# Performance work log

Hardware: AMD Instinct MI355X
Metric: run time of the kernel (lower is better)

## Reference

```python
import jax, jax.numpy as jnp
import numpy as np

B = 4096
C3 = 1.0 / np.sqrt(3.0)
# Wigner 3j tensors for the l<=1 paths (e3nn real basis)
W3J_000 = jnp.ones((1, 1, 1), dtype=jnp.float32)
W3J_110 = (jnp.eye(3) * C3).reshape(3, 3, 1).astype(jnp.float32)
W3J_011 = (jnp.eye(3) * C3).reshape(1, 3, 3).astype(jnp.float32)
W3J_101 = (jnp.eye(3) * C3).reshape(3, 1, 3).astype(jnp.float32)


def setup_inputs() -> dict:
    key = jax.random.key(0)
    ks = jax.random.split(key, 10)
    n = lambda k, s: jax.random.normal(k, s, dtype=jnp.float32)
    return {
        "feat": n(ks[0], (B, 320)),        # 128x0e + 64x1o
        "node_emb": n(ks[1], (B, 128)),
        # o3.Linear(irreps_node -> irreps_block): one mixing matrix per l
        "W0": n(ks[2], (128, 16)),          # 0e: 128 -> 16
        "W1": n(ks[3], (64, 16)),           # 1o: 64 -> 16
        # lin_weight MLP: 128 -> 64 -> 36864
        "lw1": n(ks[4], (128, 64)) * 0.1, "lb1": jnp.zeros((64,), jnp.float32),
        "lw2": n(ks[5], (64, 36864)) * 0.1, "lb2": jnp.zeros((36864,), jnp.float32),
        # lin_bias MLP: 128 -> 64 -> 1280
        "bw1": n(ks[6], (128, 64)) * 0.1, "bb1": jnp.zeros((64,), jnp.float32),
        "bw2": n(ks[7], (64, 1280)) * 0.1, "bb2": jnp.zeros((1280,), jnp.float32),
    }


def _path(x, wpath, w3j, bias):
    # x: [B, mul_in, dim_in]; wpath: [B, mul_in, u, v]; w3j: [i, j, k]
    r = jnp.einsum('bwuv,bwk->buvk', wpath, x)
    if bias is not None:
        r = r + bias[..., None]
    out = jnp.einsum('ijk,buvk->buivj', w3j, r) / x.shape[1]
    b, u, i, v, j = out.shape
    return out.reshape(b, u * i, v * j)


def reference(feat, node_emb, W0, W1, lw1, lb1, lw2, lb2, bw1, bb1, bw2, bb2):
    bn = feat.shape[0]
    # split feat into irreps: 128x0e | 64x1o
    s = feat[:, :128].reshape(bn, 128, 1)
    v = feat[:, 128:].reshape(bn, 64, 3)
    # o3.Linear with e3nn path normalization 1/sqrt(fan_in)
    x0 = jnp.einsum('buk,uv->bvk', s, W0) / np.sqrt(128.0)  # [B,16,1]
    x1 = jnp.einsum('buk,uv->bvk', v, W1) / np.sqrt(64.0)   # [B,16,3]
    # per-sample path weights and biases
    w = jax.nn.silu(node_emb @ lw1 + lb1) @ lw2 + lb2        # [B,36864]
    bb = jax.nn.silu(node_emb @ bw1 + bb1) @ bw2 + bb2       # [B,1280]
    # weight slices per instruction (flat layout matches instruction order)
    w00 = w[:, :16384].reshape(bn, 16, 32, 32)               # 0e -> (0e,0e)
    w11 = w[:, 16384:20480].reshape(bn, 16, 16, 16)          # 0e -> (1o,1o)
    w01 = w[:, 20480:28672].reshape(bn, 16, 32, 16)          # 1o -> (0e,1o)
    w10 = w[:, 28672:36864].reshape(bn, 16, 16, 32)          # 1o -> (1o,0e)
    b00 = bb[:, :1024].reshape(bn, 32, 32)
    b11 = bb[:, 1024:1280].reshape(bn, 16, 16)
    blk00 = _path(x0, w00, W3J_000, b00)   # [B,32,32]
    blk11 = _path(x0, w11, W3J_110, b11)   # [B,48,48]
    blk01 = _path(x1, w01, W3J_011, None)  # [B,32,48]
    blk10 = _path(x1, w10, W3J_101, None)  # [B,48,32]
    top = jnp.concatenate([blk00, blk01], axis=-1)
    bot = jnp.concatenate([blk10, blk11], axis=-1)
    return jnp.concatenate([top, bot], axis=-2)  # [B,80,80]
```

## Files before the change

kernel.cpp:

```cpp
#include <hip/hip_runtime.h>
#include <hip/hip_bf16.h>
#include <math.h>


typedef short bf16x8 __attribute__((ext_vector_type(8)));
typedef float f32x4 __attribute__((ext_vector_type(4)));

static __device__ __forceinline__ short f2bf(float f) {
  unsigned u = __builtin_bit_cast(unsigned, f);
  u = u + 0x7fffu + ((u >> 16) & 1u);
  return (short)(u >> 16);
}

__global__ void k_transpose(const float* __restrict__ lw2, short* __restrict__ lw2f) {
  __shared__ float tile[64][65];
  int n0 = blockIdx.x * 64;
  int t = threadIdx.x;
#pragma unroll
  for (int k = 0; k < 16; ++k) {
    int idx = k * 256 + t;
    int c = idx >> 6, j = idx & 63;
    tile[c][j] = lw2[(size_t)c * 36864 + n0 + j];
  }
  __syncthreads();
#pragma unroll
  for (int k = 0; k < 16; ++k) {
    int idx = k * 256 + t;
    int e = idx & 7, l = (idx >> 3) & 63, half = (idx >> 9) & 1, nbl = idx >> 10;
    int q = l >> 4, colr = l & 15;
    int j = nbl * 16 + colr;
    int c = half * 32 + q * 8 + e;
    size_t nb = (size_t)(n0 >> 4) + nbl;
    lw2f[((nb * 2 + half) * 64 + l) * 8 + e] = f2bf(tile[c][j]);
  }
}

__global__ void k_bias(const float* __restrict__ bw2, const float* __restrict__ lb2,
                       const float* __restrict__ bb2,
                       short* __restrict__ bbf00, short* __restrict__ bbf11,
                       short* __restrict__ bbf01, short* __restrict__ bbf10) {
  int i = blockIdx.x * 256 + threadIdx.x;
  if (i < 98304) {
    int uvb = i / 1536, r = i % 1536;
    int kk = r >> 9, l = (r >> 3) & 63, e = r & 7;
    int q = l >> 4, col = l & 15;
    int uv = uvb * 16 + col, k = kk * 32 + q * 8 + e;
    float v = 0.0f;
    if (k < 64) v = bw2[k * 1280 + uv];
    else if (k < 80) v = lb2[(k - 64) * 1024 + uv];
    else if (k == 80) v = bb2[uv];
    bbf00[i] = f2bf(v);
  } else if (i < 122880) {
    int j = i - 98304;
    int uvb = j / 1536, r = j % 1536;
    int kk = r >> 9, l = (r >> 3) & 63, e = r & 7;
    int q = l >> 4, col = l & 15;
    int uv = uvb * 16 + col, k = kk * 32 + q * 8 + e;
    float v = 0.0f;
    if (k < 64) v = bw2[k * 1280 + 1024 + uv];
    else if (k < 80) v = lb2[16384 + (k - 64) * 256 + uv];
    else if (k == 80) v = bb2[1024 + uv];
    bbf11[j] = f2bf(v);
  } else if (i < 139264) {
    int j = i - 122880;
    int uvb = j >> 9, r = j & 511;
    int l = (r >> 3) & 63, e = r & 7;
    int q = l >> 4, col = l & 15;
    int uv = uvb * 16 + col, k = q * 8 + e;
    bbf01[j] = (k < 16) ? f2bf(lb2[20480 + k * 512 + uv]) : (short)0;
  } else if (i < 155648) {
    int j = i - 139264;
    int uvb = j >> 9, r = j & 511;
    int l = (r >> 3) & 63, e = r & 7;
    int q = l >> 4, col = l & 15;
    int uv = uvb * 16 + col, k = q * 8 + e;
    bbf10[j] = (k < 16) ? f2bf(lb2[28672 + k * 512 + uv]) : (short)0;
  }
}

__global__ void k_samples(const float* __restrict__ feat, const float* __restrict__ ne,
                          const float* __restrict__ W0, const float* __restrict__ W1,
                          const float* __restrict__ lw1, const float* __restrict__ lb1,
                          const float* __restrict__ bw1, const float* __restrict__ bb1,
                          float* __restrict__ H, float* __restrict__ H2,
                          float* __restrict__ X0, float* __restrict__ X1) {
  int b = blockIdx.x;
  int t = threadIdx.x;
  __shared__ float sne[128];
  __shared__ float sf[320];
  if (t < 128) sne[t] = ne[(size_t)b * 128 + t];
  for (int i = t; i < 320; i += 192) sf[i] = feat[(size_t)b * 320 + i];
  __syncthreads();
  if (t < 64) {
    float a = lb1[t];
    for (int k = 0; k < 128; ++k) a += sne[k] * lw1[k * 64 + t];
    H[(size_t)b * 64 + t] = a / (1.0f + expf(-a));
  } else if (t < 128) {
    int c = t - 64;
    float a = bb1[c];
    for (int k = 0; k < 128; ++k) a += sne[k] * bw1[k * 64 + c];
    H2[(size_t)b * 64 + c] = a / (1.0f + expf(-a));
  } else if (t < 144) {
    int v = t - 128;
    float a = 0.0f;
    for (int u = 0; u < 128; ++u) a += sf[u] * W0[u * 16 + v];
    X0[(size_t)b * 16 + v] = a * 0.08838834764831845f;
  } else {
    int idx = t - 144, v = idx / 3, j = idx % 3;
    float a = 0.0f;
    for (int u = 0; u < 64; ++u) a += sf[128 + u * 3 + j] * W1[u * 16 + v];
    X1[(size_t)b * 48 + v * 3 + j] = a * 0.125f;
  }
}

__global__ void k_q(const float* __restrict__ H, const float* __restrict__ H2,
                    const float* __restrict__ X0, const float* __restrict__ X1,
                    short* __restrict__ QF, short* __restrict__ AbF,
                    short* __restrict__ A1F) {
  int bid = blockIdx.x;
  int g16 = bid >> 3, part = bid & 7;
  int b0 = g16 * 16;
  int t = threadIdx.x;
  __shared__ float sH[16][64];
  __shared__ float sH2[16][64];
  __shared__ float sX0[16][16];
  __shared__ float sX1[16][48];
  for (int i = t; i < 1024; i += 256) {
    sH [i >> 6][i & 63] = H [(size_t)(b0 + (i >> 6)) * 64 + (i & 63)];
    sH2[i >> 6][i & 63] = H2[(size_t)(b0 + (i >> 6)) * 64 + (i & 63)];
  }
  sX0[t >> 4][t & 15] = X0[(size_t)(b0 + (t >> 4)) * 16 + (t & 15)];
  for (int i = t; i < 768; i += 256)
    sX1[i / 48][i % 48] = X1[(size_t)(b0 + i / 48) * 48 + (i % 48)];
  __syncthreads();
#pragma unroll
  for (int it = 0; it < 16; ++it) {
    int i = part * 4096 + it * 256 + t;
    int p = i >> 13, rem = i & 8191;
    int kk = rem >> 8, lane = (rem >> 2) & 63, e2 = (rem & 3) << 1;
    int cc = lane & 15, q = lane >> 4;
    int k = kk * 32 + q * 8 + e2;
    int w = k >> 6, c = k & 63;
    float xw = (p == 0) ? sX0[cc][w] : sX1[cc][w * 3 + (p - 1)];
    unsigned lo = (unsigned short)f2bf(sH[cc][c] * xw);
    unsigned hi = (unsigned short)f2bf(sH[cc][c + 1] * xw);
    ((unsigned*)QF)[(size_t)g16 * 32768 + i] = lo | (hi << 16);
  }
  if (part == 0) {
    for (int i = t; i < 1536; i += 256) {
      int kk = i >> 9, lane = (i >> 3) & 63, e = i & 7;
      int cc = lane & 15, q = lane >> 4;
      int k = kk * 32 + q * 8 + e;
      float v = 0.0f;
      if (k < 64) v = sH2[cc][k];
      else if (k < 80) v = sX0[cc][k - 64];
      else if (k == 80) v = 1.0f;
      AbF[(size_t)g16 * 1536 + i] = f2bf(v);
    }
  } else if (part == 1) {
    for (int i = t; i < 1536; i += 256) {
      int j = i >> 9, r = i & 511;
      int lane = r >> 3, e = r & 7;
      int cc = lane & 15, q = lane >> 4;
      int k = q * 8 + e;
      A1F[(size_t)g16 * 1536 + i] = (k < 16) ? f2bf(sX1[cc][k * 3 + j]) : (short)0;
    }
  }
}

template <int NP, int N, int NB16, int NS16>
static __device__ __forceinline__ void mm_stream(
    const short* __restrict__ LW2F, const short* __restrict__ sQ0,
    int uvb, int lane8, f32x4 (&acc)[NP][N]) {
  auto bptr = [&](int kk, int i) -> const bf16x8* {
    return (const bf16x8*)(LW2F +
        ((size_t)(NB16 + (kk >> 1) * NS16 + uvb + i) * 2 + (kk & 1)) * 512 + lane8);
  };
  bf16x8 B[2][N];
#pragma unroll
  for (int d = 0; d < 2; ++d)
#pragma unroll
    for (int i = 0; i < N; ++i) B[d][i] = *bptr(d, i);
#pragma unroll
  for (int kk = 0; kk < 32; ++kk) {
    const int d = kk & 1;
    bf16x8 A[NP];
#pragma unroll
    for (int p = 0; p < NP; ++p)
      A[p] = *(const bf16x8*)(sQ0 + p * 16384 + kk * 512 + lane8);
#pragma unroll
    for (int i = 0; i < N; ++i)
#pragma unroll
      for (int p = 0; p < NP; ++p)
        acc[p][i] = __builtin_amdgcn_mfma_f32_16x16x32_bf16(A[p], B[d][i], acc[p][i], 0, 0, 0);
    if (kk + 2 < 32) {
#pragma unroll
      for (int i = 0; i < N; ++i) B[d][i] = *bptr(kk + 2, i);
    }
  }
}

template <int NP, int N, int NBIAS>
static __device__ __forceinline__ void mm_bias(
    const short* __restrict__ BBF, const short* __restrict__ Ab0, int astride,
    int uvb, int lane8, f32x4 (&acc)[NP][N]) {
#pragma unroll
  for (int kk = 0; kk < NBIAS; ++kk)
#pragma unroll
    for (int i = 0; i < N; ++i) {
      const bf16x8 Bx = *(const bf16x8*)(BBF + (size_t)((uvb + i) * NBIAS + kk) * 512 + lane8);
#pragma unroll
      for (int p = 0; p < NP; ++p) {
        const bf16x8 Ap = *(const bf16x8*)(Ab0 + p * astride + kk * 512 + lane8);
        acc[p][i] = __builtin_amdgcn_mfma_f32_16x16x32_bf16(Ap, Bx, acc[p][i], 0, 0, 0);
      }
    }
}

__global__ __launch_bounds__(1024, 1)
__attribute__((amdgpu_num_vgpr(128)))
void k_main(
    const short* __restrict__ LW2F,
    const short* __restrict__ BBF00, const short* __restrict__ BBF11,
    const short* __restrict__ BBF01, const short* __restrict__ BBF10,
    const short* __restrict__ QF, const short* __restrict__ AbF,
    const short* __restrict__ A1F, float* __restrict__ out) {
  constexpr float S00 = 0.0625f;
  constexpr float S3 = 0.036084391824351614f;

  int bidx = blockIdx.x;
  int xslot = bidx & 7;
  int h = xslot >> 2;
  int s = (xslot & 3) + 4 * (bidx >> 3);
  int b0 = s << 5;
  int t = threadIdx.x;
  int lane = t & 63, slot = t >> 6;
  int col = lane & 15, q = lane >> 4;
  int lane8 = lane * 8;

  __shared__ short sQ[4 * 16384];
  __shared__ short sAb[2 * 1536];
  __shared__ short sA1[6 * 512];

  for (int i = t; i < 384; i += 1024) {
    int g = i >= 192, r = i - g * 192;
    ((uint4*)(sAb + g * 1536))[r] =
        ((const uint4*)(AbF + (size_t)(s * 2 + g) * 1536))[r];
  }
  for (int i = t; i < 384; i += 1024) {
    int jp = i >> 6, r = i & 63;
    int j = jp >> 1, g = jp & 1;
    ((uint4*)(sA1 + jp * 512))[r] =
        ((const uint4*)(A1F + ((size_t)(s * 2 + g) * 3 + j) * 512))[r];
  }
  for (int i = t; i < 4096; i += 1024) {
    int pl = i >> 11, r = i & 2047;
    const uint4* src = (const uint4*)(QF + (size_t)(s * 2 + pl) * 65536);
    ((uint4*)sQ)[pl * 2048 + r] = src[r];
  }
  __syncthreads();

  {
    int uvb = h * 32 + slot * 2;
    f32x4 acc[2][2] = {};
    mm_stream<2, 2, 0, 64>(LW2F, sQ, uvb, lane8, acc);
    mm_bias<2, 2, 3>(BBF00, sAb, 1536, uvb, lane8, acc);
#pragma unroll
    for (int g = 0; g < 2; ++g)
#pragma unroll
      for (int i = 0; i < 2; ++i)
#pragma unroll
        for (int ii = 0; ii < 4; ++ii) {
          size_t ob = (size_t)(b0 + g * 16 + q * 4 + ii) * 6400;
          int uv = (uvb + i) * 16 + col;
          out[ob + (uv >> 5) * 80 + (uv & 31)] = acc[g][i][ii] * S00;
        }
  }
  if (slot < 8) {
    int uvb = h * 8 + slot;
    f32x4 acc[2][1] = {};
    mm_stream<2, 1, 1024, 16>(LW2F, sQ, uvb, lane8, acc);
    mm_bias<2, 1, 3>(BBF11, sAb, 1536, uvb, lane8, acc);
#pragma unroll
    for (int g = 0; g < 2; ++g)
#pragma unroll
      for (int ii = 0; ii < 4; ++ii) {
        size_t ob = (size_t)(b0 + g * 16 + q * 4 + ii) * 6400;
        int uv = uvb * 16 + col;
        float val = acc[g][0][ii] * S3;
        int u = uv >> 4, v = uv & 15;
        float* p = out + ob + (size_t)(32 + 3 * u) * 80 + (32 + 3 * v);
        p[0] = val;   p[1] = 0.f;   p[2] = 0.f;
        p[80] = 0.f;  p[81] = val;  p[82] = 0.f;
        p[160] = 0.f; p[161] = 0.f; p[162] = val;
      }
  }

  __syncthreads();
  for (int i = t; i < 8192; i += 1024) {
    int pl = i >> 11, r = i & 2047;
    const uint4* src = (const uint4*)(QF +
        ((size_t)(s * 2 + (pl & 1)) * 4 + 1 + (pl >> 1)) * 16384);
    ((uint4*)sQ)[pl * 2048 + r] = src[r];
  }
  __syncthreads();
  {
    int uvb = h * 16 + slot;
    {
      f32x4 acc[4][1] = {};
      mm_stream<4, 1, 1280, 32>(LW2F, sQ, uvb, lane8, acc);
      mm_bias<4, 1, 1>(BBF01, sA1, 512, uvb, lane8, acc);
#pragma unroll
      for (int p = 0; p < 4; ++p)
#pragma unroll
        for (int ii = 0; ii < 4; ++ii) {
          int j = p >> 1, g = p & 1;
          size_t ob = (size_t)(b0 + g * 16 + q * 4 + ii) * 6400;
          int uv = uvb * 16 + col;
          out[ob + (uv >> 4) * 80 + 32 + 3 * (uv & 15) + j] = acc[p][0][ii] * S3;
        }
    }
    {
      f32x4 acc[4][1] = {};
      mm_stream<4, 1, 1792, 32>(LW2F, sQ, uvb, lane8, acc);
      mm_bias<4, 1, 1>(BBF10, sA1, 512, uvb, lane8, acc);
#pragma unroll
      for (int p = 0; p < 4; ++p)
#pragma unroll
        for (int ii = 0; ii < 4; ++ii) {
          int j = p >> 1, g = p & 1;
          size_t ob = (size_t)(b0 + g * 16 + q * 4 + ii) * 6400;
          int uv = uvb * 16 + col;
          out[ob + (size_t)(32 + 3 * (uv >> 5) + j) * 80 + (uv & 31)] = acc[p][0][ii] * S3;
        }
    }
  }

  __syncthreads();
  for (int i = t; i < 4096; i += 1024) {
    int pl = i >> 11, r = i & 2047;
    const uint4* src = (const uint4*)(QF + ((size_t)(s * 2 + pl) * 4 + 3) * 16384);
    ((uint4*)sQ)[pl * 2048 + r] = src[r];
  }
  __syncthreads();
  {
    int uvb = h * 16 + slot;
    {
      f32x4 acc[2][1] = {};
      mm_stream<2, 1, 1280, 32>(LW2F, sQ, uvb, lane8, acc);
      mm_bias<2, 1, 1>(BBF01, sA1 + 4 * 512, 512, uvb, lane8, acc);
#pragma unroll
      for (int g = 0; g < 2; ++g)
#pragma unroll
        for (int ii = 0; ii < 4; ++ii) {
          size_t ob = (size_t)(b0 + g * 16 + q * 4 + ii) * 6400;
          int uv = uvb * 16 + col;
          out[ob + (uv >> 4) * 80 + 32 + 3 * (uv & 15) + 2] = acc[g][0][ii] * S3;
        }
    }
    {
      f32x4 acc[2][1] = {};
      mm_stream<2, 1, 1792, 32>(LW2F, sQ, uvb, lane8, acc);
      mm_bias<2, 1, 1>(BBF10, sA1 + 4 * 512, 512, uvb, lane8, acc);
#pragma unroll
      for (int g = 0; g < 2; ++g)
#pragma unroll
        for (int ii = 0; ii < 4; ++ii) {
          size_t ob = (size_t)(b0 + g * 16 + q * 4 + ii) * 6400;
          int uv = uvb * 16 + col;
          out[ob + (size_t)(32 + 3 * (uv >> 5) + 2) * 80 + (uv & 31)] = acc[g][0][ii] * S3;
        }
    }
  }
}

extern "C" void kernel_launch(void* const* d_in, const int* in_sizes, int n_in,
                              void* d_out, int out_size, void* d_ws, size_t ws_size,
                              hipStream_t stream) {
  const float* feat = (const float*)d_in[0];
  const float* ne   = (const float*)d_in[1];
  const float* W0   = (const float*)d_in[2];
  const float* W1   = (const float*)d_in[3];
  const float* lw1  = (const float*)d_in[4];
  const float* lb1  = (const float*)d_in[5];
  const float* lw2  = (const float*)d_in[6];
  const float* lb2  = (const float*)d_in[7];
  const float* bw1  = (const float*)d_in[8];
  const float* bb1  = (const float*)d_in[9];
  const float* bw2  = (const float*)d_in[10];
  const float* bb2  = (const float*)d_in[11];

  char* ws = (char*)d_ws;
  short* LW2F  = (short*)ws; ws += (size_t)36864 * 64 * 2;
  short* BBF00 = (short*)ws; ws += (size_t)98304 * 2;
  short* BBF11 = (short*)ws; ws += (size_t)24576 * 2;
  short* BBF01 = (short*)ws; ws += (size_t)16384 * 2;
  short* BBF10 = (short*)ws; ws += (size_t)16384 * 2;
  float* H  = (float*)ws;   ws += (size_t)4096 * 64 * 4;
  float* H2 = (float*)ws;   ws += (size_t)4096 * 64 * 4;
  float* X0 = (float*)ws;   ws += (size_t)4096 * 16 * 4;
  float* X1 = (float*)ws;   ws += (size_t)4096 * 48 * 4;
  short* QF  = (short*)ws;  ws += (size_t)256 * 65536 * 2;
  short* AbF = (short*)ws;  ws += (size_t)256 * 1536 * 2;
  short* A1F = (short*)ws;  ws += (size_t)256 * 1536 * 2;
  (void)ws_size; (void)in_sizes; (void)n_in; (void)out_size;

  hipLaunchKernelGGL(k_transpose, dim3(576), dim3(256), 0, stream, lw2, LW2F);
  hipLaunchKernelGGL(k_bias, dim3(608), dim3(256), 0, stream, bw2, lb2, bb2,
                     BBF00, BBF11, BBF01, BBF10);
  hipLaunchKernelGGL(k_samples, dim3(4096), dim3(192), 0, stream,
                     feat, ne, W0, W1, lw1, lb1, bw1, bb1, H, H2, X0, X1);
  hipLaunchKernelGGL(k_q, dim3(2048), dim3(256), 0, stream,
                     H, H2, X0, X1, QF, AbF, A1F);
  hipLaunchKernelGGL(k_main, dim3(256), dim3(1024), 0, stream,
                     LW2F, BBF00, BBF11, BBF01, BBF10, QF, AbF, A1F, (float*)d_out);
}
```

Before: 142.1 us.

## Split main kernel into separate l=0-input and l=1-input path kernels

Splits the monolithic main kernel into two launches. The first handles the 00 and 11 paths with 16-sample tiles over 512 blocks and a smaller shared-memory footprint. The second handles the 01 and 10 paths with the original 32-sample tiling. This is meant to raise parallelism and occupancy for the first phase and drop the mid-kernel reload barrier. The cost is an extra kernel launch and halved reuse of streamed LW2F weights per block in the first phase.

```diff
diff --git a/kernel.cpp b/kernel.cpp
--- a/kernel.cpp
+++ b/kernel.cpp
@@ -217,15 +217,70 @@
     }
 }
 
-__global__ __launch_bounds__(1024, 1)
-__attribute__((amdgpu_num_vgpr(128)))
-void k_main(
+__global__ __launch_bounds__(1024, 1) void k_mainA(
     const short* __restrict__ LW2F,
     const short* __restrict__ BBF00, const short* __restrict__ BBF11,
+    const short* __restrict__ QF, const short* __restrict__ AbF,
+    float* __restrict__ out) {
+  constexpr float S00 = 0.0625f;
+  constexpr float S3 = 0.036084391824351614f;
+
+  int bidx = blockIdx.x;
+  int xslot = bidx & 7;
+  int h = xslot >> 2;
+  int tile = (xslot & 3) + 4 * (bidx >> 3);
+  int b0 = tile << 4;
+  int t = threadIdx.x;
+  int lane = t & 63, slot = t >> 6;
+  int col = lane & 15, q = lane >> 4;
+  int lane8 = lane * 8;
+
+  __shared__ short sQ[16384];
+  __shared__ short sAb[1536];
+
+  for (int i = t; i < 2048; i += 1024)
+    ((uint4*)sQ)[i] = ((const uint4*)(QF + (size_t)tile * 65536))[i];
+  if (t < 192) ((uint4*)sAb)[t] = ((const uint4*)(AbF + (size_t)tile * 1536))[t];
+  __syncthreads();
+
+  {
+    int uvb = h * 32 + slot * 2;
+    f32x4 acc[1][2] = {};
+    mm_stream<1, 2, 0, 64>(LW2F, sQ, uvb, lane8, acc);
+    mm_bias<1, 2, 3>(BBF00, sAb, 1536, uvb, lane8, acc);
+#pragma unroll
+    for (int i = 0; i < 2; ++i)
+#pragma unroll
+      for (int ii = 0; ii < 4; ++ii) {
+        size_t ob = (size_t)(b0 + q * 4 + ii) * 6400;
+        int uv = (uvb + i) * 16 + col;
+        out[ob + (uv >> 5) * 80 + (uv & 31)] = acc[0][i][ii] * S00;
+      }
+  }
+  if (slot < 8) {
+    int uvb = h * 8 + slot;
+    f32x4 acc[1][1] = {};
+    mm_stream<1, 1, 1024, 16>(LW2F, sQ, uvb, lane8, acc);
+    mm_bias<1, 1, 3>(BBF11, sAb, 1536, uvb, lane8, acc);
+#pragma unroll
+    for (int ii = 0; ii < 4; ++ii) {
+      size_t ob = (size_t)(b0 + q * 4 + ii) * 6400;
+      int uv = uvb * 16 + col;
+      float val = acc[0][0][ii] * S3;
+      int u = uv >> 4, v = uv & 15;
+      float* p = out + ob + (size_t)(32 + 3 * u) * 80 + (32 + 3 * v);
+      p[0] = val;   p[1] = 0.f;   p[2] = 0.f;
+      p[80] = 0.f;  p[81] = val;  p[82] = 0.f;
+      p[160] = 0.f; p[161] = 0.f; p[162] = val;
+    }
+  }
+}
+
+__global__ __launch_bounds__(1024, 1) void k_mainB(
+    const short* __restrict__ LW2F,
     const short* __restrict__ BBF01, const short* __restrict__ BBF10,
-    const short* __restrict__ QF, const short* __restrict__ AbF,
-    const short* __restrict__ A1F, float* __restrict__ out) {
-  constexpr float S00 = 0.0625f;
+    const short* __restrict__ QF, const short* __restrict__ A1F,
+    float* __restrict__ out) {
   constexpr float S3 = 0.036084391824351614f;
 
   int bidx = blockIdx.x;
@@ -239,64 +294,14 @@
   int lane8 = lane * 8;
 
   __shared__ short sQ[4 * 16384];
-  __shared__ short sAb[2 * 1536];
   __shared__ short sA1[6 * 512];
 
-  for (int i = t; i < 384; i += 1024) {
-    int g = i >= 192, r = i - g * 192;
-    ((uint4*)(sAb + g * 1536))[r] =
-        ((const uint4*)(AbF + (size_t)(s * 2 + g) * 1536))[r];
-  }
   for (int i = t; i < 384; i += 1024) {
     int jp = i >> 6, r = i & 63;
     int j = jp >> 1, g = jp & 1;
     ((uint4*)(sA1 + jp * 512))[r] =
         ((const uint4*)(A1F + ((size_t)(s * 2 + g) * 3 + j) * 512))[r];
   }
-  for (int i = t; i < 4096; i += 1024) {
-    int pl = i >> 11, r = i & 2047;
-    const uint4* src = (const uint4*)(QF + (size_t)(s * 2 + pl) * 65536);
-    ((uint4*)sQ)[pl * 2048 + r] = src[r];
-  }
-  __syncthreads();
-
-  {
-    int uvb = h * 32 + slot * 2;
-    f32x4 acc[2][2] = {};
-    mm_stream<2, 2, 0, 64>(LW2F, sQ, uvb, lane8, acc);
-    mm_bias<2, 2, 3>(BBF00, sAb, 1536, uvb, lane8, acc);
-#pragma unroll
-    for (int g = 0; g < 2; ++g)
-#pragma unroll
-      for (int i = 0; i < 2; ++i)
-#pragma unroll
-        for (int ii = 0; ii < 4; ++ii) {
-          size_t ob = (size_t)(b0 + g * 16 + q * 4 + ii) * 6400;
-          int uv = (uvb + i) * 16 + col;
-          out[ob + (uv >> 5) * 80 + (uv & 31)] = acc[g][i][ii] * S00;
-        }
-  }
-  if (slot < 8) {
-    int uvb = h * 8 + slot;
-    f32x4 acc[2][1] = {};
-    mm_stream<2, 1, 1024, 16>(LW2F, sQ, uvb, lane8, acc);
-    mm_bias<2, 1, 3>(BBF11, sAb, 1536, uvb, lane8, acc);
-#pragma unroll
-    for (int g = 0; g < 2; ++g)
-#pragma unroll
-      for (int ii = 0; ii < 4; ++ii) {
-        size_t ob = (size_t)(b0 + g * 16 + q * 4 + ii) * 6400;
-        int uv = uvb * 16 + col;
-        float val = acc[g][0][ii] * S3;
-        int u = uv >> 4, v = uv & 15;
-        float* p = out + ob + (size_t)(32 + 3 * u) * 80 + (32 + 3 * v);
-        p[0] = val;   p[1] = 0.f;   p[2] = 0.f;
-        p[80] = 0.f;  p[81] = val;  p[82] = 0.f;
-        p[160] = 0.f; p[161] = 0.f; p[162] = val;
-      }
-  }
-
-  __syncthreads();
   for (int i = t; i < 8192; i += 1024) {
     int pl = i >> 11, r = i & 2047;
     const uint4* src = (const uint4*)(QF +
@@ -412,6 +417,8 @@
                      feat, ne, W0, W1, lw1, lb1, bw1, bb1, H, H2, X0, X1);
   hipLaunchKernelGGL(k_q, dim3(2048), dim3(256), 0, stream,
                      H, H2, X0, X1, QF, AbF, A1F);
-  hipLaunchKernelGGL(k_main, dim3(256), dim3(1024), 0, stream,
-                     LW2F, BBF00, BBF11, BBF01, BBF10, QF, AbF, A1F, (float*)d_out);
-}
+  hipLaunchKernelGGL(k_mainA, dim3(512), dim3(1024), 0, stream,
+                     LW2F, BBF00, BBF11, QF, AbF, (float*)d_out);
+  hipLaunchKernelGGL(k_mainB, dim3(256), dim3(1024), 0, stream,
+                     LW2F, BBF01, BBF10, QF, A1F, (float*)d_out);
+}
```

Result: slower. 173.4 us (+22.0%).
